# Performance work log

Hardware: AMD Instinct MI355X
Metric: run time of the kernel (lower is better)

The kernel has to match this reference:

```python
import jax, jax.numpy as jnp
import numpy as np
from jax import lax

FEAT_STRIDE = 16
SCALES = np.array([8.0, 16.0, 32.0])
RATIOS = np.array([0.5, 1.0, 2.0])
PRE_NMS_TOPN = 6000
POST_NMS_TOPN = 300
NMS_THRESH = 0.7


def _whctrs(a):
    w = a[2] - a[0] + 1.0
    h = a[3] - a[1] + 1.0
    return w, h, a[0] + 0.5 * (w - 1.0), a[1] + 0.5 * (h - 1.0)


def _mkanchors(ws, hs, xc, yc):
    return np.stack([xc - 0.5 * (ws - 1.0), yc - 0.5 * (hs - 1.0),
                     xc + 0.5 * (ws - 1.0), yc + 0.5 * (hs - 1.0)], axis=1)


def generate_anchors(base_size=16):
    base = np.array([0.0, 0.0, base_size - 1.0, base_size - 1.0])
    w, h, xc, yc = _whctrs(base)
    size = w * h
    ws = np.round(np.sqrt(size / RATIOS))
    hs = np.round(ws * RATIOS)
    ratio_anchors = _mkanchors(ws, hs, np.full_like(ws, xc), np.full_like(ws, yc))
    out = []
    for a in ratio_anchors:
        w, h, xc, yc = _whctrs(a)
        out.append(_mkanchors(w * SCALES, h * SCALES,
                              np.full_like(SCALES, xc), np.full_like(SCALES, yc)))
    return np.concatenate(out, axis=0).astype(np.float32)  # (A=9, 4)


def _pairwise_iou(boxes):
    x1, y1, x2, y2 = boxes[:, 0], boxes[:, 1], boxes[:, 2], boxes[:, 3]
    area = (x2 - x1 + 1.0) * (y2 - y1 + 1.0)
    iw = jnp.maximum(0.0, jnp.minimum(x2[:, None], x2[None, :]) - jnp.maximum(x1[:, None], x1[None, :]) + 1.0)
    ih = jnp.maximum(0.0, jnp.minimum(y2[:, None], y2[None, :]) - jnp.maximum(y1[:, None], y1[None, :]) + 1.0)
    inter = iw * ih
    return inter / (area[:, None] + area[None, :] - inter)


def _nms_keep(iou, thresh):
    n = iou.shape[0]
    idx = jnp.arange(n)
    def body(keep, i):
        suppress = keep[i] & (iou[i] > thresh) & (idx > i)
        return keep & (~suppress), None
    keep, _ = lax.scan(body, jnp.ones((n,), dtype=bool), idx)
    return keep


def _per_image(props, sc):
    # descending score sort, keep top pre_nms
    order = jnp.argsort(-sc)[:PRE_NMS_TOPN]
    boxes = props[order]  # (PRE, 4)
    iou = _pairwise_iou(boxes)  # (PRE, PRE)
    keep = _nms_keep(iou, NMS_THRESH)
    rank = jnp.cumsum(keep) - 1
    valid = keep & (rank < POST_NMS_TOPN)
    slot = jnp.where(valid, rank, POST_NMS_TOPN)  # dump invalid into spare slot
    out = jnp.zeros((POST_NMS_TOPN + 1, 4), boxes.dtype)
    out = out.at[slot].set(jnp.where(valid[:, None], boxes, 0.0))
    return out[:POST_NMS_TOPN]


def reference(scores, bbox_deltas, im_info):
    B, C2, H, W = scores.shape
    A = C2 // 2
    anchors = jnp.asarray(generate_anchors())  # (A, 4)
    sx = (jnp.arange(W) * FEAT_STRIDE).astype(jnp.float32)
    sy = (jnp.arange(H) * FEAT_STRIDE).astype(jnp.float32)
    gy, gx = jnp.meshgrid(sy, sx, indexing='ij')
    shifts = jnp.stack([gx.ravel(), gy.ravel(), gx.ravel(), gy.ravel()], axis=1)  # (K, 4)
    all_anchors = (anchors[None, :, :] + shifts[:, None, :]).reshape(-1, 4)  # (K*A, 4)

    deltas = bbox_deltas.transpose(0, 2, 3, 1).reshape(B, -1, 4)  # (B, K*A, 4)
    sc = scores[:, A:].transpose(0, 2, 3, 1).reshape(B, -1)        # (B, K*A)

    # bbox_transform_inv
    wa = all_anchors[:, 2] - all_anchors[:, 0] + 1.0
    ha = all_anchors[:, 3] - all_anchors[:, 1] + 1.0
    cxa = all_anchors[:, 0] + 0.5 * wa
    cya = all_anchors[:, 1] + 0.5 * ha
    dx, dy, dw, dh = deltas[..., 0], deltas[..., 1], deltas[..., 2], deltas[..., 3]
    pcx = dx * wa + cxa
    pcy = dy * ha + cya
    pw = jnp.exp(dw) * wa
    ph = jnp.exp(dh) * ha
    x1 = pcx - 0.5 * pw
    y1 = pcy - 0.5 * ph
    x2 = pcx + 0.5 * pw
    y2 = pcy + 0.5 * ph

    # clip_boxes
    im_h = im_info[:, 0:1]
    im_w = im_info[:, 1:2]
    x1 = jnp.clip(x1, 0.0, im_w - 1.0)
    x2 = jnp.clip(x2, 0.0, im_w - 1.0)
    y1 = jnp.clip(y1, 0.0, im_h - 1.0)
    y2 = jnp.clip(y2, 0.0, im_h - 1.0)
    props = jnp.stack([x1, y1, x2, y2], axis=-1)  # (B, K*A, 4)

    out_boxes = jax.vmap(_per_image)(props, sc)  # (B, POST, 4)
    batch_idx = jnp.broadcast_to(
        jnp.arange(B, dtype=out_boxes.dtype)[:, None, None], (B, POST_NMS_TOPN, 1))
    return jnp.concatenate([batch_idx, out_boxes], axis=-1)  # (B, POST, 5)


def setup_inputs() -> dict:
    key = jax.random.key(0)
    k1, k2 = jax.random.split(key)
    B, A, H, W = 4, 9, 50, 76
    scores = jax.random.uniform(k1, (B, 2 * A, H, W), dtype=jnp.float32)
    bbox_deltas = jax.random.normal(k2, (B, 4 * A, H, W), dtype=jnp.float32) * 0.1
    im_info = jnp.ones((B, 3), jnp.float32) * jnp.array([800.0, 1216.0, 1.0], jnp.float32)
    return {"scores": scores, "bbox_deltas": bbox_deltas, "im_info": im_info}
```

## Files before the change

kernel.cpp:

```cpp
#include <hip/hip_runtime.h>
#include <stdint.h>

#define B_     4
#define A_     9
#define H_     50
#define W_     76
#define HW_    (H_ * W_)
#define N_     (HW_ * A_)
#define PRE_   6000
#define POST_  300
#define NBIN   16384
#define BINOFF 0xC000
#define SKCAP  8192
#define ACTMAX 256
#define FXCAP  2048
#define NB_    94

__constant__ float c_anchors[9][4] = {
    { -84.f,  -40.f,  99.f,  55.f},
    {-176.f,  -88.f, 191.f, 103.f},
    {-360.f, -184.f, 375.f, 199.f},
    { -56.f,  -56.f,  71.f,  71.f},
    {-120.f, -120.f, 135.f, 135.f},
    {-248.f, -248.f, 263.f, 263.f},
    { -36.f,  -80.f,  51.f,  95.f},
    { -80.f, -168.f,  95.f, 183.f},
    {-168.f, -344.f, 183.f, 359.f},
};

__device__ __forceinline__ int sb_bin(unsigned int sb) {
    int bin = (int)((~sb) >> 16) - BINOFF;
    return bin < 0 ? 0 : bin;
}

__global__ __launch_bounds__(1024) void k_hps(const float* __restrict__ scores,
                                              unsigned long long* __restrict__ skeys,
                                              unsigned int* __restrict__ actA,
                                              unsigned int* __restrict__ actB,
                                              unsigned int* __restrict__ actcnt) {
    const int b = blockIdx.x, tid = threadIdx.x;
    const int lane = tid & 63, wid = tid >> 6;
    __shared__ unsigned int LHIST[NBIN];
    __shared__ unsigned int s_wsum[16];
    __shared__ unsigned int s_aA[ACTMAX];
    __shared__ unsigned int s_aB[ACTMAX];
    __shared__ int s_actn, s_binhi;

    for (int i = tid; i < NBIN; i += 1024) LHIST[i] = 0u;
    if (tid == 0) { s_actn = 0; s_binhi = 0; }
    __syncthreads();

    const float* sc = scores + (size_t)((b * 2 * A_) + A_) * HW_;
    for (int i = tid; i < N_; i += 1024) {
        unsigned int sb = __float_as_uint(sc[i]);
        atomicAdd(&LHIST[sb_bin(sb)], 1u);
    }
    __syncthreads();

    {
        int base0 = tid * 16;
        unsigned int sum = 0;
        for (int q = 0; q < 16; ++q) sum += LHIST[base0 + q];
        unsigned int inc = sum;
#pragma unroll
        for (int off = 1; off < 64; off <<= 1) {
            unsigned int t = __shfl_up(inc, off);
            if (lane >= off) inc += t;
        }
        if (lane == 63) s_wsum[wid] = inc;
        __syncthreads();
        unsigned int wbase = 0;
        for (int wq = 0; wq < wid; ++wq) wbase += s_wsum[wq];
        unsigned int run = wbase + inc - sum;
        int mybinhi = -1;
        for (int q = 0; q < 16; ++q) {
            unsigned int c = LHIST[base0 + q];
            LHIST[base0 + q] = run;
            if (run < (unsigned int)PRE_) {
                mybinhi = base0 + q;
                if (c > 0) {
                    int pos = atomicAdd(&s_actn, 1);
                    if (pos < ACTMAX) {
                        s_aA[pos] = run;
                        s_aB[pos] = ((unsigned int)(base0 + q) << 16) | (c & 0xffffu);
                    }
                }
            }
            run += c;
        }
        if (mybinhi >= 0) atomicMax(&s_binhi, mybinhi);
    }
    __syncthreads();

    {
        int binhi = s_binhi;
        for (int i = tid; i < N_; i += 1024) {
            unsigned int sb = __float_as_uint(sc[i]);
            int bin = sb_bin(sb);
            if (bin <= binhi) {
                unsigned int slot = atomicAdd(&LHIST[bin], 1u);
                if (slot < SKCAP) {
                    int a = i / HW_, r = i - a * HW_;
                    unsigned int n = (unsigned int)(r * A_ + a);
                    skeys[b * SKCAP + slot] =
                        (((unsigned long long)(~sb)) << 32) | (unsigned long long)n;
                }
            }
        }
    }
    int n = s_actn; if (n > ACTMAX) n = ACTMAX;
    for (int i = tid; i < n; i += 1024) {
        actA[b * ACTMAX + i] = s_aA[i];
        actB[b * ACTMAX + i] = s_aB[i];
    }
    if (tid == 0) actcnt[b] = (unsigned int)n;
}

__device__ __forceinline__ void compute_box(int b, unsigned int n,
                                            const float* __restrict__ deltas,
                                            const float* __restrict__ im_info,
                                            float box[4]) {
#pragma clang fp contract(off)
    int a   = (int)(n % A_);
    int pos = (int)(n / A_);
    int w   = pos % W_;
    int h   = pos / W_;
    float a0 = c_anchors[a][0] + (float)(w * 16);
    float a1 = c_anchors[a][1] + (float)(h * 16);
    float a2 = c_anchors[a][2] + (float)(w * 16);
    float a3 = c_anchors[a][3] + (float)(h * 16);
    float wa  = a2 - a0 + 1.f;
    float ha  = a3 - a1 + 1.f;
    float cxa = a0 + 0.5f * wa;
    float cya = a1 + 0.5f * ha;
    int base = ((b * 4 * A_ + a * 4) * H_ + h) * W_ + w;
    const int chs = HW_;
    float dx = deltas[base];
    float dy = deltas[base + chs];
    float dw = deltas[base + 2 * chs];
    float dh = deltas[base + 3 * chs];
    float pcx = dx * wa + cxa;
    float pcy = dy * ha + cya;
    float pw  = expf(dw) * wa;
    float ph  = expf(dh) * ha;
    float x1 = pcx - 0.5f * pw;
    float y1 = pcy - 0.5f * ph;
    float x2 = pcx + 0.5f * pw;
    float y2 = pcy + 0.5f * ph;
    float imh = im_info[b * 3 + 0], imw = im_info[b * 3 + 1];
    x1 = fminf(fmaxf(x1, 0.f), imw - 1.f);
    x2 = fminf(fmaxf(x2, 0.f), imw - 1.f);
    y1 = fminf(fmaxf(y1, 0.f), imh - 1.f);
    y2 = fminf(fmaxf(y2, 0.f), imh - 1.f);
    box[0] = x1; box[1] = y1; box[2] = x2; box[3] = y2;
}

__global__ __launch_bounds__(256) void k_fixup(const unsigned long long* __restrict__ skeys,
                                               const unsigned int* __restrict__ actA,
                                               const unsigned int* __restrict__ actB,
                                               const unsigned int* __restrict__ actcnt,
                                               const float* __restrict__ deltas,
                                               const float* __restrict__ im_info,
                                               float* __restrict__ sboxes) {
    int b = blockIdx.y;
    unsigned int nact = actcnt[b];
    if (nact > ACTMAX) nact = ACTMAX;
    if (blockIdx.x >= nact) return;
    int tid = threadIdx.x;
    unsigned int start = actA[b * ACTMAX + blockIdx.x];
    unsigned int ab    = actB[b * ACTMAX + blockIdx.x];
    unsigned int cnt   = ab & 0xffffu;
    unsigned int m = cnt;
    if (start + m > SKCAP) m = SKCAP - start;
    if (m > FXCAP) m = FXCAP;
    __shared__ unsigned long long lk[FXCAP];
    for (unsigned int i = tid; i < m; i += 256) lk[i] = skeys[b * SKCAP + start + i];
    __syncthreads();
    float4* sb4 = (float4*)sboxes;
    for (unsigned int e = tid; e < m; e += 256) {
        unsigned long long k = lk[e];
        unsigned int r = 0;
        for (unsigned int i = 0; i < m; ++i) r += (lk[i] < k) ? 1u : 0u;
        unsigned int pos = start + r;
        if (pos < (unsigned int)PRE_) {
            unsigned int n = (unsigned int)(k & 0xffffffffull);
            float box[4];
            compute_box(b, n, deltas, im_info, box);
            sb4[b * PRE_ + pos] = make_float4(box[0], box[1], box[2], box[3]);
        }
    }
}

__device__ __forceinline__ bool iou_gt(float4 p, float pa, float4 q, float qa) {
    float iw = fminf(p.z, q.z) - fmaxf(p.x, q.x) + 1.f;
    float ih = fminf(p.w, q.w) - fmaxf(p.y, q.y) + 1.f;
    iw = fmaxf(iw, 0.f); ih = fmaxf(ih, 0.f);
    float inter = iw * ih;
    float iou = inter / ((pa + qa) - inter);
    return iou > 0.7f;
}

__global__ __launch_bounds__(1024) void k_nms(const float* __restrict__ sboxes,
                                              float* __restrict__ out) {
    int b = blockIdx.x;
    int tid = threadIdx.x;
    int lane = tid & 63;
    int wave = tid >> 6;
    __shared__ float4 s_box[POST_ + 64];
    __shared__ float  s_ar [POST_ + 64];
    __shared__ unsigned long long s_pend[2][16];
    __shared__ unsigned long long s_mtile[3][64];
    __shared__ int s_cnt[2];
    __shared__ int s_final;
    if (tid < 32) ((unsigned long long*)s_pend)[tid] = 0ull;
    if (tid < 2) s_cnt[tid] = 0;
    if (tid == 0) s_final = 0;

    const float4* bb = (const float4*)sboxes + b * PRE_;
    float* ob = out + b * POST_ * 5;

    {
        int blk01 = (wave < 8) ? 0 : 1;
        int wrel = wave & 7;
        float4 vb = bb[blk01 * 64 + lane];
        float ab = ((vb.z - vb.x) + 1.f) * ((vb.w - vb.y) + 1.f);
        for (int r = wrel * 8; r < wrel * 8 + 8; ++r) {
            float4 p;
            p.x = __shfl(vb.x, r); p.y = __shfl(vb.y, r);
            p.z = __shfl(vb.z, r); p.w = __shfl(vb.w, r);
            float pa = __shfl(ab, r);
            unsigned long long bal = __ballot((lane > r) && iou_gt(p, pa, vb, ab));
            if (lane == 0) s_mtile[blk01][r] = bal;
        }
    }
    float4 vme;
    if (wave == 0) vme = bb[lane];
    else           vme = bb[64 + lane];
    __syncthreads();

    for (int k = 0; k < NB_; ++k) {
        int Cm1 = s_cnt[(k + 1) & 1];
        if (Cm1 >= POST_) break;
        if (wave == 0) {
            int idx = k * 64 + lane;
            bool valid = idx < PRE_;
            float4 v = vme;
            unsigned long long row = s_mtile[k % 3][lane];
            if (k + 1 < NB_) {
                int nidx = (k + 1) * 64 + lane;
                vme = bb[nidx < PRE_ ? nidx : PRE_ - 1];
            }
            float area = ((v.z - v.x) + 1.f) * ((v.w - v.y) + 1.f);
            int Cm2 = s_cnt[k & 1];
            bool sup = !valid;
            int kk = Cm2;
            for (; kk + 1 < Cm1; kk += 2) {
                float4 k0 = s_box[kk],   k1 = s_box[kk + 1];
                float  r0 = s_ar [kk],   r1 = s_ar [kk + 1];
                sup = sup | iou_gt(v, area, k0, r0) | iou_gt(v, area, k1, r1);
            }
            for (; kk < Cm1; ++kk)
                sup = sup | iou_gt(v, area, s_box[kk], s_ar[kk]);
            unsigned long long supm = __ballot(sup);
            const unsigned long long* pnd = s_pend[k & 1];
#pragma unroll
            for (int w2 = 1; w2 < 16; ++w2) supm |= pnd[w2];
            unsigned int rlo = (unsigned int)row;
            unsigned int rhi = (unsigned int)(row >> 32);
            unsigned long long alive = ~supm;
            unsigned long long keepm = 0ull;
            while (alive) {
                int i = __builtin_ctzll(alive);
                keepm |= (1ull << i);
                alive &= ~(1ull << i);
                unsigned long long mlo = (unsigned int)__builtin_amdgcn_readlane((int)rlo, i);
                unsigned long long mhi = (unsigned int)__builtin_amdgcn_readlane((int)rhi, i);
                alive &= ~((mhi << 32) | mlo);
            }
            if ((keepm >> lane) & 1ull) {
                int my = Cm1 + __builtin_popcountll(keepm & ((1ull << lane) - 1ull));
                s_box[my] = v;
                s_ar [my] = area;
                if (my < POST_) {
                    ob[my * 5 + 0] = (float)b;
                    ob[my * 5 + 1] = v.x; ob[my * 5 + 2] = v.y;
                    ob[my * 5 + 3] = v.z; ob[my * 5 + 4] = v.w;
                }
            }
            if (lane == 0) {
                int nc = Cm1 + __builtin_popcountll(keepm);
                s_cnt[k & 1] = nc;
                s_final = nc;
            }
        } else if (k + 1 < NB_) {
            int jdx = (k + 1) * 64 + lane;
            bool valid2 = jdx < PRE_;
            float4 v2 = vme;
            if (k + 2 < NB_) {
                int nj = (k + 2) * 64 + lane;
                vme = bb[nj < PRE_ ? nj : PRE_ - 1];
            }
            float area2 = ((v2.z - v2.x) + 1.f) * ((v2.w - v2.y) + 1.f);
            bool sup2 = !valid2;
            int kk = wave - 1;
            for (; kk + 45 < Cm1; kk += 60) {
                float4 k0 = s_box[kk],      k1 = s_box[kk + 15];
                float4 k2 = s_box[kk + 30], k3 = s_box[kk + 45];
                float  r0 = s_ar [kk],      r1 = s_ar [kk + 15];
                float  r2 = s_ar [kk + 30], r3 = s_ar [kk + 45];
                sup2 = sup2 | iou_gt(v2, area2, k0, r0) | iou_gt(v2, area2, k1, r1)
                            | iou_gt(v2, area2, k2, r2) | iou_gt(v2, area2, k3, r3);
            }
            for (; kk < Cm1; kk += 15)
                sup2 = sup2 | iou_gt(v2, area2, s_box[kk], s_ar[kk]);
            unsigned long long bal = __ballot(sup2);
            if (lane == 0) s_pend[(k + 1) & 1][wave] = bal;
            if (k + 2 < NB_) {
                float amex = ((vme.z - vme.x) + 1.f) * ((vme.w - vme.y) + 1.f);
                int slot = (k + 2) % 3;
                for (int r = wave - 1; r < 64; r += 15) {
                    float4 p;
                    p.x = __shfl(vme.x, r); p.y = __shfl(vme.y, r);
                    p.z = __shfl(vme.z, r); p.w = __shfl(vme.w, r);
                    float pa = __shfl(amex, r);
                    unsigned long long mb = __ballot((lane > r) && iou_gt(p, pa, vme, amex));
                    if (lane == 0) s_mtile[slot][r] = mb;
                }
            }
        }
        __syncthreads();
    }
    __syncthreads();
    int kept = s_final;
    int start = kept < POST_ ? kept : POST_;
    for (int r = start + tid; r < POST_; r += 1024) {
        ob[r * 5 + 0] = (float)b;
        ob[r * 5 + 1] = 0.f; ob[r * 5 + 2] = 0.f;
        ob[r * 5 + 3] = 0.f; ob[r * 5 + 4] = 0.f;
    }
}

extern "C" void kernel_launch(void* const* d_in, const int* in_sizes, int n_in,
                              void* d_out, int out_size, void* d_ws, size_t ws_size,
                              hipStream_t stream) {
    const float* scores  = (const float*)d_in[0];
    const float* deltas  = (const float*)d_in[1];
    const float* im_info = (const float*)d_in[2];
    float* out = (float*)d_out;

    char* ws = (char*)d_ws;
    unsigned long long* skeys  = (unsigned long long*)(ws);
    unsigned int*       actA   = (unsigned int*)      (ws + 262144);
    unsigned int*       actB   = (unsigned int*)      (ws + 266240);
    unsigned int*       actcnt = (unsigned int*)      (ws + 270336);
    float*              sbx    = (float*)             (ws + 270368);

    k_hps<<<B_, 1024, 0, stream>>>(scores, skeys, actA, actB, actcnt);
    dim3 fgrid(ACTMAX, B_);
    k_fixup<<<fgrid, 256, 0, stream>>>(skeys, actA, actB, actcnt, deltas, im_info, sbx);
    k_nms<<<B_, 1024, 0, stream>>>(sbx, out);
}
```

Before: 81.74 us.

## Fuse histogram selection and bin fixup into one kernel with LDS keys

Merges the histogram/partition kernel and the per-bin rank fixup kernel into a single per-image block. Keys stay in shared memory instead of a global workspace, and each wave ranks one active bin using register-held keys and wave shuffles. This removes a kernel launch and the global key traffic. In exchange, the fixup that ran on a wide grid now runs on only four blocks, with large LDS use per block.

```diff
diff --git a/kernel.cpp b/kernel.cpp
--- a/kernel.cpp
+++ b/kernel.cpp
@@ -13,7 +13,7 @@
 #define BINOFF 0xC000
 #define SKCAP  8192
 #define ACTMAX 256
-#define FXCAP  2048
+#define KCAP   256
 #define NB_    94
 
 __constant__ float c_anchors[9][4] = {
@@ -31,89 +31,6 @@
 __device__ __forceinline__ int sb_bin(unsigned int sb) {
     int bin = (int)((~sb) >> 16) - BINOFF;
     return bin < 0 ? 0 : bin;
-}
-
-__global__ __launch_bounds__(1024) void k_hps(const float* __restrict__ scores,
-                                              unsigned long long* __restrict__ skeys,
-                                              unsigned int* __restrict__ actA,
-                                              unsigned int* __restrict__ actB,
-                                              unsigned int* __restrict__ actcnt) {
-    const int b = blockIdx.x, tid = threadIdx.x;
-    const int lane = tid & 63, wid = tid >> 6;
-    __shared__ unsigned int LHIST[NBIN];
-    __shared__ unsigned int s_wsum[16];
-    __shared__ unsigned int s_aA[ACTMAX];
-    __shared__ unsigned int s_aB[ACTMAX];
-    __shared__ int s_actn, s_binhi;
-
-    for (int i = tid; i < NBIN; i += 1024) LHIST[i] = 0u;
-    if (tid == 0) { s_actn = 0; s_binhi = 0; }
-    __syncthreads();
-
-    const float* sc = scores + (size_t)((b * 2 * A_) + A_) * HW_;
-    for (int i = tid; i < N_; i += 1024) {
-        unsigned int sb = __float_as_uint(sc[i]);
-        atomicAdd(&LHIST[sb_bin(sb)], 1u);
-    }
-    __syncthreads();
-
-    {
-        int base0 = tid * 16;
-        unsigned int sum = 0;
-        for (int q = 0; q < 16; ++q) sum += LHIST[base0 + q];
-        unsigned int inc = sum;
-#pragma unroll
-        for (int off = 1; off < 64; off <<= 1) {
-            unsigned int t = __shfl_up(inc, off);
-            if (lane >= off) inc += t;
-        }
-        if (lane == 63) s_wsum[wid] = inc;
-        __syncthreads();
-        unsigned int wbase = 0;
-        for (int wq = 0; wq < wid; ++wq) wbase += s_wsum[wq];
-        unsigned int run = wbase + inc - sum;
-        int mybinhi = -1;
-        for (int q = 0; q < 16; ++q) {
-            unsigned int c = LHIST[base0 + q];
-            LHIST[base0 + q] = run;
-            if (run < (unsigned int)PRE_) {
-                mybinhi = base0 + q;
-                if (c > 0) {
-                    int pos = atomicAdd(&s_actn, 1);
-                    if (pos < ACTMAX) {
-                        s_aA[pos] = run;
-                        s_aB[pos] = ((unsigned int)(base0 + q) << 16) | (c & 0xffffu);
-                    }
-                }
-            }
-            run += c;
-        }
-        if (mybinhi >= 0) atomicMax(&s_binhi, mybinhi);
-    }
-    __syncthreads();
-
-    {
-        int binhi = s_binhi;
-        for (int i = tid; i < N_; i += 1024) {
-            unsigned int sb = __float_as_uint(sc[i]);
-            int bin = sb_bin(sb);
-            if (bin <= binhi) {
-                unsigned int slot = atomicAdd(&LHIST[bin], 1u);
-                if (slot < SKCAP) {
-                    int a = i / HW_, r = i - a * HW_;
-                    unsigned int n = (unsigned int)(r * A_ + a);
-                    skeys[b * SKCAP + slot] =
-                        (((unsigned long long)(~sb)) << 32) | (unsigned long long)n;
-                }
-            }
-        }
-    }
-    int n = s_actn; if (n > ACTMAX) n = ACTMAX;
-    for (int i = tid; i < n; i += 1024) {
-        actA[b * ACTMAX + i] = s_aA[i];
-        actB[b * ACTMAX + i] = s_aB[i];
-    }
-    if (tid == 0) actcnt[b] = (unsigned int)n;
 }
 
 __device__ __forceinline__ void compute_box(int b, unsigned int n,
@@ -155,38 +72,139 @@
     box[0] = x1; box[1] = y1; box[2] = x2; box[3] = y2;
 }
 
-__global__ __launch_bounds__(256) void k_fixup(const unsigned long long* __restrict__ skeys,
-                                               const unsigned int* __restrict__ actA,
-                                               const unsigned int* __restrict__ actB,
-                                               const unsigned int* __restrict__ actcnt,
-                                               const float* __restrict__ deltas,
-                                               const float* __restrict__ im_info,
-                                               float* __restrict__ sboxes) {
-    int b = blockIdx.y;
-    unsigned int nact = actcnt[b];
-    if (nact > ACTMAX) nact = ACTMAX;
-    if (blockIdx.x >= nact) return;
-    int tid = threadIdx.x;
-    unsigned int start = actA[b * ACTMAX + blockIdx.x];
-    unsigned int ab    = actB[b * ACTMAX + blockIdx.x];
-    unsigned int cnt   = ab & 0xffffu;
-    unsigned int m = cnt;
-    if (start + m > SKCAP) m = SKCAP - start;
-    if (m > FXCAP) m = FXCAP;
-    __shared__ unsigned long long lk[FXCAP];
-    for (unsigned int i = tid; i < m; i += 256) lk[i] = skeys[b * SKCAP + start + i];
-    __syncthreads();
-    float4* sb4 = (float4*)sboxes;
-    for (unsigned int e = tid; e < m; e += 256) {
-        unsigned long long k = lk[e];
-        unsigned int r = 0;
-        for (unsigned int i = 0; i < m; ++i) r += (lk[i] < k) ? 1u : 0u;
-        unsigned int pos = start + r;
-        if (pos < (unsigned int)PRE_) {
-            unsigned int n = (unsigned int)(k & 0xffffffffull);
-            float box[4];
-            compute_box(b, n, deltas, im_info, box);
-            sb4[b * PRE_ + pos] = make_float4(box[0], box[1], box[2], box[3]);
+__global__ __launch_bounds__(1024) void k_hps_fx(const float* __restrict__ scores,
+                                                 const float* __restrict__ deltas,
+                                                 const float* __restrict__ im_info,
+                                                 float* __restrict__ sboxes) {
+    const int b = blockIdx.x, tid = threadIdx.x;
+    const int lane = tid & 63, wid = tid >> 6;
+    __shared__ unsigned int LHIST[NBIN];
+    __shared__ unsigned long long SKEY[SKCAP];
+    __shared__ unsigned int s_wsum[16];
+    __shared__ unsigned int s_aA[ACTMAX];
+    __shared__ unsigned int s_aB[ACTMAX];
+    __shared__ int s_actn, s_binhi;
+
+    for (int i = tid; i < NBIN; i += 1024) LHIST[i] = 0u;
+    if (tid == 0) { s_actn = 0; s_binhi = 0; }
+    __syncthreads();
+
+    const float* sc = scores + (size_t)((b * 2 * A_) + A_) * HW_;
+    for (int i = tid; i < N_; i += 1024) {
+        unsigned int sb = __float_as_uint(sc[i]);
+        atomicAdd(&LHIST[sb_bin(sb)], 1u);
+    }
+    __syncthreads();
+
+    {
+        int base0 = tid * 16;
+        unsigned int sum = 0;
+        for (int q = 0; q < 16; ++q) sum += LHIST[base0 + q];
+        unsigned int inc = sum;
+#pragma unroll
+        for (int off = 1; off < 64; off <<= 1) {
+            unsigned int t = __shfl_up(inc, off);
+            if (lane >= off) inc += t;
+        }
+        if (lane == 63) s_wsum[wid] = inc;
+        __syncthreads();
+        unsigned int wbase = 0;
+        for (int wq = 0; wq < wid; ++wq) wbase += s_wsum[wq];
+        unsigned int run = wbase + inc - sum;
+        int mybinhi = -1;
+        for (int q = 0; q < 16; ++q) {
+            unsigned int c = LHIST[base0 + q];
+            LHIST[base0 + q] = run;
+            if (run < (unsigned int)PRE_) {
+                mybinhi = base0 + q;
+                if (c > 0) {
+                    int pos = atomicAdd(&s_actn, 1);
+                    if (pos < ACTMAX) {
+                        s_aA[pos] = run;
+                        s_aB[pos] = ((unsigned int)(base0 + q) << 16) | (c & 0xffffu);
+                    }
+                }
+            }
+            run += c;
+        }
+        if (mybinhi >= 0) atomicMax(&s_binhi, mybinhi);
+    }
+    __syncthreads();
+
+    {
+        int binhi = s_binhi;
+        for (int i = tid; i < N_; i += 1024) {
+            unsigned int sb = __float_as_uint(sc[i]);
+            int bin = sb_bin(sb);
+            if (bin <= binhi) {
+                unsigned int slot = atomicAdd(&LHIST[bin], 1u);
+                if (slot < SKCAP) {
+                    int a = i / HW_, r = i - a * HW_;
+                    unsigned int n = (unsigned int)(r * A_ + a);
+                    SKEY[slot] =
+                        (((unsigned long long)(~sb)) << 32) | (unsigned long long)n;
+                }
+            }
+        }
+    }
+    __syncthreads();
+
+    {
+        int nact = s_actn; if (nact > ACTMAX) nact = ACTMAX;
+        float4* sb4 = (float4*)sboxes;
+        for (int t = wid; t < nact; t += 16) {
+            unsigned int start = s_aA[t];
+            unsigned int m     = s_aB[t] & 0xffffu;
+            if (start + m > SKCAP) m = SKCAP - start;
+            const unsigned long long* kb = SKEY + start;
+            if (m <= KCAP) {
+                unsigned long long kreg[4];
+                unsigned int rnk[4];
+#pragma unroll
+                for (int q = 0; q < 4; ++q) {
+                    unsigned int e = (unsigned int)lane + q * 64u;
+                    kreg[q] = (e < m) ? kb[e] : ~0ull;
+                    rnk[q] = 0;
+                }
+#pragma unroll
+                for (int q2 = 0; q2 < 4; ++q2) {
+                    int base2 = q2 * 64;
+                    if (base2 >= (int)m) break;
+                    unsigned long long kq = kreg[q2];
+                    int lim = (int)m - base2; if (lim > 64) lim = 64;
+                    for (int l = 0; l < lim; ++l) {
+                        unsigned long long ki = __shfl(kq, l);
+#pragma unroll
+                        for (int q = 0; q < 4; ++q) rnk[q] += (ki < kreg[q]) ? 1u : 0u;
+                    }
+                }
+#pragma unroll
+                for (int q = 0; q < 4; ++q) {
+                    unsigned int e = (unsigned int)lane + q * 64u;
+                    if (e < m) {
+                        unsigned int pos = start + rnk[q];
+                        if (pos < (unsigned int)PRE_) {
+                            unsigned int n = (unsigned int)(kreg[q] & 0xffffffffull);
+                            float box[4];
+                            compute_box(b, n, deltas, im_info, box);
+                            sb4[b * PRE_ + pos] = make_float4(box[0], box[1], box[2], box[3]);
+                        }
+                    }
+                }
+            } else {
+                for (unsigned int e = lane; e < m; e += 64) {
+                    unsigned long long k = kb[e];
+                    unsigned int r = 0;
+                    for (unsigned int i2 = 0; i2 < m; ++i2) r += (kb[i2] < k) ? 1u : 0u;
+                    unsigned int pos = start + r;
+                    if (pos < (unsigned int)PRE_) {
+                        unsigned int n = (unsigned int)(k & 0xffffffffull);
+                        float box[4];
+                        compute_box(b, n, deltas, im_info, box);
+                        sb4[b * PRE_ + pos] = make_float4(box[0], box[1], box[2], box[3]);
+                    }
+                }
+            }
         }
     }
 }
@@ -348,15 +366,8 @@
     const float* im_info = (const float*)d_in[2];
     float* out = (float*)d_out;
 
-    char* ws = (char*)d_ws;
-    unsigned long long* skeys  = (unsigned long long*)(ws);
-    unsigned int*       actA   = (unsigned int*)      (ws + 262144);
-    unsigned int*       actB   = (unsigned int*)      (ws + 266240);
-    unsigned int*       actcnt = (unsigned int*)      (ws + 270336);
-    float*              sbx    = (float*)             (ws + 270368);
-
-    k_hps<<<B_, 1024, 0, stream>>>(scores, skeys, actA, actB, actcnt);
-    dim3 fgrid(ACTMAX, B_);
-    k_fixup<<<fgrid, 256, 0, stream>>>(skeys, actA, actB, actcnt, deltas, im_info, sbx);
+    float* sbx = (float*)d_ws;
+
+    k_hps_fx<<<B_, 1024, 0, stream>>>(scores, deltas, im_info, sbx);
     k_nms<<<B_, 1024, 0, stream>>>(sbx, out);
 }
```

After: 117.8 us. +44.2%, slower.
